# Performance work log

Measured on AMD Instinct MI355X. Metric: run time of the kernel, lower is better.

Reference implementation:

```python
import jax, jax.numpy as jnp
import numpy as np

D_MODEL = 1024
N_HEADS = 16
WINDOW = 256
CAUSAL = True


def build_sliding_window_mask(T, window_size, causal=True):
    half = window_size // 2
    i = jnp.arange(T)[:, None]
    j = jnp.arange(T)[None, :]
    attend = jnp.abs(i - j) <= half
    if causal:
        attend = attend & (j <= i)
    return jnp.where(attend, 0.0, -jnp.inf).astype(jnp.float32)  # (T, T)


def setup_inputs() -> dict:
    key = jax.random.key(0)
    kx, kq, kk, kv, ko = jax.random.split(key, 5)
    B, T, D = 2, 2048, D_MODEL
    s = 1.0 / np.sqrt(D)
    return {
        "x": jax.random.normal(kx, (B, T, D), jnp.float32),
        "Wq": jax.random.normal(kq, (D, D), jnp.float32) * s,
        "Wk": jax.random.normal(kk, (D, D), jnp.float32) * s,
        "Wv": jax.random.normal(kv, (D, D), jnp.float32) * s,
        "Wo": jax.random.normal(ko, (D, D), jnp.float32) * s,
    }


def reference(x, Wq, Wk, Wv, Wo):
    B, T, D = x.shape
    H = N_HEADS
    dh = D // H
    # torch nn.Linear: y = x @ W.T
    def proj(W):
        return (x @ W.T).reshape(B, T, H, dh).transpose(0, 2, 1, 3)  # (B,H,T,dh)

    q, k, v = proj(Wq), proj(Wk), proj(Wv)
    scale = jnp.sqrt(jnp.asarray(dh, x.dtype))
    scores = jnp.einsum("bhtd,bhsd->bhts", q, k) / scale  # (B,H,T,T)
    mask = build_sliding_window_mask(T, WINDOW, CAUSAL)
    scores = scores + mask[None, None]
    attn = jax.nn.softmax(scores, axis=-1)
    attn = jnp.nan_to_num(attn, nan=0.0)
    out = jnp.einsum("bhts,bhsd->bhtd", attn, v)  # (B,H,T,dh)
    out = out.transpose(0, 2, 1, 3).reshape(B, T, D)
    return out @ Wo.T
```

## Files before the change

### kernel.cpp

```cpp
#include <hip/hip_runtime.h>
#include <hip/hip_bf16.h>

#define B_  2
#define T_  2048
#define D_  1024
#define H_  16
#define DH_ 64
#define M_  (B_ * T_)

typedef short s16x8 __attribute__((ext_vector_type(8)));
typedef float f32x4 __attribute__((ext_vector_type(4)));

__device__ inline float bfu(unsigned short u) {
    union { unsigned int i; float f; } c; c.i = ((unsigned int)u) << 16; return c.f;
}
__device__ inline unsigned short f2bf(float f) {
    union { float f; unsigned int i; } c; c.f = f;
    unsigned int r = c.i + 0x7fffu + ((c.i >> 16) & 1u);
    return (unsigned short)(r >> 16);
}
__device__ inline void stv(float* p, float v) { __builtin_nontemporal_store(v, p); }
__device__ inline void stv(unsigned short* p, float v) { *p = f2bf(v); }

__device__ inline void gload_lds16(const unsigned short* g, unsigned short* l) {
    __builtin_amdgcn_global_load_lds(
        (const __attribute__((address_space(1))) void*)g,
        (__attribute__((address_space(3))) void*)l, 16, 0, 0);
}

__global__ __launch_bounds__(256) void conv_bf16(const float* __restrict__ x,
                                                 const float* __restrict__ Wq,
                                                 const float* __restrict__ Wk,
                                                 const float* __restrict__ Wv,
                                                 const float* __restrict__ Wo,
                                                 unsigned short* __restrict__ dst) {
    for (int g = blockIdx.x * 256 + threadIdx.x; g < (1 << 21); g += 2048 * 256) {
        const float* s; size_t o;
        if (g < (1 << 20)) { s = x; o = (size_t)g; }
        else {
            int gg = g - (1 << 20);
            int w = gg >> 18;
            o = (size_t)(gg & ((1 << 18) - 1));
            s = (w == 0) ? Wq : (w == 1) ? Wk : (w == 2) ? Wv : Wo;
        }
        float4 v = ((const float4*)s)[o];
        ushort4 u;
        u.x = f2bf(v.x); u.y = f2bf(v.y); u.z = f2bf(v.z); u.w = f2bf(v.w);
        ((ushort4*)dst)[g] = u;
    }
}

template <int BM, int BN, int NH, typename Tout>
__global__ __launch_bounds__(256, 4) void gemm_m97(const unsigned short* __restrict__ A,
                                                   const unsigned short* __restrict__ Bw,
                                                   Tout* __restrict__ C0,
                                                   Tout* __restrict__ C1,
                                                   unsigned short* __restrict__ vtr,
                                                   int K) {
    constexpr int MI = BM / 32;
    constexpr int NI = BN / 32;
    __shared__ unsigned short As[NH * BM * 32];
    __shared__ unsigned short Bs[NH * BN * 32];
    const int tid  = threadIdx.x;
    const int lane = tid & 63;
    const int wave = tid >> 6;
    const int wr = wave >> 1, wc = wave & 1;

    const int gx  = gridDim.x;
    const int nwg = gx * gridDim.y;
    const int hw  = blockIdx.x + gx * blockIdx.y;
    const int l   = (hw & 7) * (nwg >> 3) + (hw >> 3);
    const int bxl = l % gx, byl = l / gx;
    const int bm = byl * BM, bn = bxl * BN;

    const int fr = lane & 15, kg = lane >> 4;
    const int lrow = lane >> 2;
    const int lcol = (lane & 3) * 8;

    f32x4 acc[MI][NI];
    #pragma unroll
    for (int mi = 0; mi < MI; ++mi)
        #pragma unroll
        for (int ni = 0; ni < NI; ++ni)
            #pragma unroll
            for (int r = 0; r < 4; ++r) acc[mi][ni][r] = 0.f;

    const unsigned short* ga = A  + (size_t)(bm + wave * 16 + lrow) * K + lcol;
    const unsigned short* gb = Bw + (size_t)(bn + wave * 16 + lrow) * K + lcol;
    unsigned short* la = &As[(wave * 16) * 32];
    unsigned short* lb = &Bs[(wave * 16) * 32];

    for (int k0 = 0; k0 < K; k0 += 32 * NH) {
        __syncthreads();
        #pragma unroll
        for (int hf = 0; hf < NH; ++hf) {
            #pragma unroll
            for (int s = 0; s < BM / 64; ++s)
                gload_lds16(ga + k0 + hf * 32 + (size_t)(s * 64) * K,
                            la + hf * BM * 32 + s * 64 * 32);
            #pragma unroll
            for (int s = 0; s < BN / 64; ++s)
                gload_lds16(gb + k0 + hf * 32 + (size_t)(s * 64) * K,
                            lb + hf * BN * 32 + s * 64 * 32);
        }
        __syncthreads();
        #pragma unroll
        for (int hf = 0; hf < NH; ++hf) {
            s16x8 af[MI], bfv[NI];
            #pragma unroll
            for (int mi = 0; mi < MI; ++mi)
                af[mi] = *(const s16x8*)&As[hf * BM * 32 + (wr * (BM / 2) + mi * 16 + fr) * 32 + kg * 8];
            #pragma unroll
            for (int ni = 0; ni < NI; ++ni)
                bfv[ni] = *(const s16x8*)&Bs[hf * BN * 32 + (wc * (BN / 2) + ni * 16 + fr) * 32 + kg * 8];
            #pragma unroll
            for (int mi = 0; mi < MI; ++mi)
                #pragma unroll
                for (int ni = 0; ni < NI; ++ni)
                    acc[mi][ni] = __builtin_amdgcn_mfma_f32_16x16x32_bf16(af[mi], bfv[ni], acc[mi][ni], 0, 0, 0);
        }
    }

    if (vtr && bn >= 2048) {
        #pragma unroll
        for (int mi = 0; mi < MI; ++mi)
            #pragma unroll
            for (int ni = 0; ni < NI; ++ni) {
                const int nl = (bn - 2048) + wc * (BN / 2) + ni * 16 + fr;
                const int h = nl >> 6, d = nl & 63;
                const int m0 = bm + wr * (BM / 2) + mi * 16 + kg * 4;
                const int b = m0 >> 11, t0 = m0 & (T_ - 1);
                ushort4 u;
                u.x = f2bf(acc[mi][ni][0]); u.y = f2bf(acc[mi][ni][1]);
                u.z = f2bf(acc[mi][ni][2]); u.w = f2bf(acc[mi][ni][3]);
                *(ushort4*)(vtr + ((size_t)(b * H_ + h) * 64 + d) * T_ + t0) = u;
            }
        return;
    }
    Tout* C = (bn < 1024) ? C0 : C1;
    const int nb = bn & 1023;
    #pragma unroll
    for (int mi = 0; mi < MI; ++mi)
        #pragma unroll
        for (int ni = 0; ni < NI; ++ni)
            #pragma unroll
            for (int r = 0; r < 4; ++r) {
                int m = bm + wr * (BM / 2) + mi * 16 + kg * 4 + r;
                int n = nb + wc * (BN / 2) + ni * 16 + fr;
                stv(&C[(size_t)m * 1024 + n], acc[mi][ni][r]);
            }
}

__global__ __launch_bounds__(256) void swa_mfma4(const unsigned short* qb,
                                                 const unsigned short* __restrict__ kb,
                                                 const unsigned short* __restrict__ vt,
                                                 unsigned short* ob) {
    __shared__ unsigned short Ks[192 * 64];
    __shared__ unsigned short Vs[64 * 208];
    const int wave = threadIdx.x >> 6;
    const int lane = threadIdx.x & 63;
    const int blk = (blockIdx.x & 7) * 128 + (blockIdx.x >> 3);
    const int i0b = (blk & 31) * 64;
    const int bh  = blk >> 5;
    const int h = bh & (H_ - 1), b = bh >> 4;
    const int g = lane >> 4, l15 = lane & 15;

    const size_t rowbase = (size_t)b * T_ * D_ + (size_t)h * DH_;
    const int klo2 = (i0b > 128) ? (i0b - 128) : 0;

    {
        const int lr = lane >> 3;
        const int gc = (lane & 7) ^ lr;
        const unsigned short* kg0 = kb + rowbase + (size_t)(klo2 + lr) * D_ + gc * 8;
        #pragma unroll
        for (int s = 0; s < 6; ++s) {
            const int i = wave * 6 + s;
            gload_lds16(kg0 + (size_t)(i * 8) * D_, &Ks[i * 8 * 64]);
        }
    }
    {
        const unsigned short* vtb = vt + (size_t)bh * 64 * T_ + klo2;
        #pragma unroll
        for (int s = 0; s < 7; ++s) {
            const int i = s * 4 + wave;
            if (i < 26) {
                const int cc = i * 64 + lane;
                const int d  = cc / 26;
                const int sl = cc - d * 26;
                const int c  = (sl < 24) ? (sl ^ (d & 7)) : sl;
                gload_lds16(vtb + (size_t)d * T_ + c * 8, &Vs[i * 512]);
            }
        }
    }

    const int i0  = i0b + wave * 16;
    const int klo = (i0 > 128) ? (i0 - 128) : 0;
    const int koff = klo - klo2;

    const unsigned short* qrow = qb + rowbase + (size_t)(i0 + l15) * D_ + g * 8;
    const s16x8 aq0 = *(const s16x8*)(qrow);
    const s16x8 aq1 = *(const s16x8*)(qrow + 32);

    __syncthreads();

    f32x4 sacc[9];
    #pragma unroll
    for (int t = 0; t < 9; ++t)
        #pragma unroll
        for (int r = 0; r < 4; ++r) sacc[t][r] = 0.f;

    #pragma unroll
    for (int t = 0; t < 9; ++t) {
        const int row = koff + t * 16 + l15;
        const int r7 = row & 7;
        s16x8 b0 = *(const s16x8*)&Ks[row * 64 + ((g     ^ r7) * 8)];
        s16x8 b1 = *(const s16x8*)&Ks[row * 64 + (((g+4) ^ r7) * 8)];
        __builtin_amdgcn_s_setprio(1);
        sacc[t] = __builtin_amdgcn_mfma_f32_16x16x32_bf16(aq0, b0, sacc[t], 0, 0, 0);
        sacc[t] = __builtin_amdgcn_mfma_f32_16x16x32_bf16(aq1, b1, sacc[t], 0, 0, 0);
        __builtin_amdgcn_s_setprio(0);
    }

    __syncthreads();
    unsigned short* Pw = &Ks[wave * (16 * 168)];
    {
        int row = lane >> 2, col = 144 + (lane & 3) * 4;
        *(uint2*)&Pw[row * 168 + col] = make_uint2(0u, 0u);
    }

    float mrow[4] = {-1e30f, -1e30f, -1e30f, -1e30f};
    #pragma unroll
    for (int t = 0; t < 9; ++t)
        #pragma unroll
        for (int r = 0; r < 4; ++r) {
            const int j  = klo + t * 16 + l15;
            const int iq = i0 + g * 4 + r;
            const bool valid = (j <= iq) && (j + 128 >= iq);
            const float s = valid ? sacc[t][r] * 0.125f : -1e30f;
            sacc[t][r] = s;
            mrow[r] = fmaxf(mrow[r], s);
        }
    #pragma unroll
    for (int r = 0; r < 4; ++r)
        #pragma unroll
        for (int off = 1; off < 16; off <<= 1)
            mrow[r] = fmaxf(mrow[r], __shfl_xor(mrow[r], off));

    float lrow[4] = {0.f, 0.f, 0.f, 0.f};
    #pragma unroll
    for (int t = 0; t < 9; ++t)
        #pragma unroll
        for (int r = 0; r < 4; ++r) {
            const float p = __expf(sacc[t][r] - mrow[r]);
            sacc[t][r] = p;
            lrow[r] += p;
        }
    #pragma unroll
    for (int r = 0; r < 4; ++r) {
        #pragma unroll
        for (int off = 1; off < 16; off <<= 1)
            lrow[r] += __shfl_xor(lrow[r], off);
    }
    float invl[4];
    #pragma unroll
    for (int r = 0; r < 4; ++r) invl[r] = 1.f / lrow[r];

    #pragma unroll
    for (int t = 0; t < 9; ++t)
        #pragma unroll
        for (int r = 0; r < 4; ++r)
            Pw[(g * 4 + r) * 168 + t * 16 + l15] = f2bf(sacc[t][r]);

    f32x4 oacc[4];
    #pragma unroll
    for (int nt = 0; nt < 4; ++nt)
        #pragma unroll
        for (int r = 0; r < 4; ++r) oacc[nt][r] = 0.f;

    const int kc0 = koff >> 3;
    #pragma unroll
    for (int kt = 0; kt < 5; ++kt) {
        const s16x8 ap = *(const s16x8*)&Pw[l15 * 168 + kt * 32 + g * 8];
        s16x8 bvv[4];
        #pragma unroll
        for (int nt = 0; nt < 4; ++nt) {
            const int d = nt * 16 + l15;
            const int c = kc0 + kt * 4 + g;
            const int sl = (c < 24) ? (c ^ (d & 7)) : c;
            bvv[nt] = *(const s16x8*)&Vs[d * 208 + sl * 8];
        }
        __builtin_amdgcn_s_setprio(1);
        #pragma unroll
        for (int nt = 0; nt < 4; ++nt)
            oacc[nt] = __builtin_amdgcn_mfma_f32_16x16x32_bf16(ap, bvv[nt], oacc[nt], 0, 0, 0);
        __builtin_amdgcn_s_setprio(0);
    }

    #pragma unroll
    for (int nt = 0; nt < 4; ++nt)
        #pragma unroll
        for (int r = 0; r < 4; ++r) {
            const float val = oacc[nt][r] * invl[r];
            ob[rowbase + (size_t)(i0 + g * 4 + r) * D_ + nt * 16 + l15] = f2bf(val);
        }
}

extern "C" void kernel_launch(void* const* d_in, const int* in_sizes, int n_in,
                              void* d_out, int out_size, void* d_ws, size_t ws_size,
                              hipStream_t stream) {
    const float* x  = (const float*)d_in[0];
    const float* Wq = (const float*)d_in[1];
    const float* Wk = (const float*)d_in[2];
    const float* Wv = (const float*)d_in[3];
    const float* Wo = (const float*)d_in[4];

    const size_t MD = (size_t)M_ * D_;
    const size_t WN = (size_t)D_ * D_;

    unsigned short* wsb = (unsigned short*)d_ws;
    unsigned short* xb  = wsb;
    unsigned short* Wqb = xb + MD;
    unsigned short* Wob = Wqb + 3 * WN;
    unsigned short* qb  = Wob + WN;
    unsigned short* vt = (unsigned short*)d_out;
    unsigned short* kb = vt + MD;

    conv_bf16<<<2048, 256, 0, stream>>>(x, Wq, Wk, Wv, Wo, wsb);

    gemm_m97<128, 128, 2, unsigned short><<<dim3(24, M_ / 128), 256, 0, stream>>>(
        xb, Wqb, qb, kb, vt, D_);

    swa_mfma4<<<(B_ * H_ * T_) / 64, 256, 0, stream>>>(qb, kb, vt, qb);

    gemm_m97<64, 128, 4, float><<<dim3(8, M_ / 64), 256, 0, stream>>>(
        qb, Wob, (float*)d_out, (float*)d_out, nullptr, D_);
}
```

Measured before the change: 140.2 us.

## Fuse all four stages into one persistent kernel with grid barriers

Replaces the four separate launches (convert, QKV GEMM, sliding-window attention, output GEMM) with one persistent kernel of 768 blocks. The stages are separated by atomic-counter grid barriers, and one shared LDS buffer is reused across stages. This removes per-launch overhead and the gaps between kernels. In exchange it adds a memset, barrier spin cost, and load imbalance, since the attention stage runs 1024 tiles over 768 blocks and the last GEMM uses only 512 blocks. It also relies on all blocks being co-resident, which is checked once through an occupancy query.

```diff
diff --git a/kernel.cpp b/kernel.cpp
--- a/kernel.cpp
+++ b/kernel.cpp
@@ -28,13 +28,27 @@
         (__attribute__((address_space(3))) void*)l, 16, 0, 0);
 }
 
-__global__ __launch_bounds__(256) void conv_bf16(const float* __restrict__ x,
-                                                 const float* __restrict__ Wq,
-                                                 const float* __restrict__ Wk,
-                                                 const float* __restrict__ Wv,
-                                                 const float* __restrict__ Wo,
-                                                 unsigned short* __restrict__ dst) {
-    for (int g = blockIdx.x * 256 + threadIdx.x; g < (1 << 21); g += 2048 * 256) {
+__device__ inline void gridbar(int* c, int nblk) {
+    __syncthreads();
+    __threadfence();
+    if (threadIdx.x == 0) {
+        int t = atomicAdd(c, 1) + 1;
+        int target = ((t + nblk - 1) / nblk) * nblk;
+        while (__hip_atomic_load(c, __ATOMIC_RELAXED, __HIP_MEMORY_SCOPE_AGENT) < target)
+            __builtin_amdgcn_s_sleep(16);
+    }
+    __syncthreads();
+    __threadfence();
+}
+
+__device__ __forceinline__ void conv_work(const float* __restrict__ x,
+                                          const float* __restrict__ Wq,
+                                          const float* __restrict__ Wk,
+                                          const float* __restrict__ Wv,
+                                          const float* __restrict__ Wo,
+                                          unsigned short* __restrict__ dst,
+                                          int nblocks) {
+    for (int g = blockIdx.x * 256 + threadIdx.x; g < (1 << 21); g += nblocks * 256) {
         const float* s; size_t o;
         if (g < (1 << 20)) { s = x; o = (size_t)g; }
         else {
@@ -50,25 +64,29 @@
     }
 }
 
+__global__ __launch_bounds__(256) void conv_bf16(const float* __restrict__ x,
+                                                 const float* __restrict__ Wq,
+                                                 const float* __restrict__ Wk,
+                                                 const float* __restrict__ Wv,
+                                                 const float* __restrict__ Wo,
+                                                 unsigned short* __restrict__ dst) {
+    conv_work(x, Wq, Wk, Wv, Wo, dst, 2048);
+}
+
 template <int BM, int BN, int NH, typename Tout>
-__global__ __launch_bounds__(256, 4) void gemm_m97(const unsigned short* __restrict__ A,
-                                                   const unsigned short* __restrict__ Bw,
-                                                   Tout* __restrict__ C0,
-                                                   Tout* __restrict__ C1,
-                                                   unsigned short* __restrict__ vtr,
-                                                   int K) {
+__device__ __forceinline__ void gemm_tile(unsigned short* As, unsigned short* Bs,
+                                          const unsigned short* __restrict__ A,
+                                          const unsigned short* __restrict__ Bw,
+                                          Tout* __restrict__ C0, Tout* __restrict__ C1,
+                                          unsigned short* __restrict__ vtr, int K,
+                                          int hw, int gx, int nwg) {
     constexpr int MI = BM / 32;
     constexpr int NI = BN / 32;
-    __shared__ unsigned short As[NH * BM * 32];
-    __shared__ unsigned short Bs[NH * BN * 32];
     const int tid  = threadIdx.x;
     const int lane = tid & 63;
     const int wave = tid >> 6;
     const int wr = wave >> 1, wc = wave & 1;
 
-    const int gx  = gridDim.x;
-    const int nwg = gx * gridDim.y;
-    const int hw  = blockIdx.x + gx * blockIdx.y;
     const int l   = (hw & 7) * (nwg >> 3) + (hw >> 3);
     const int bxl = l % gx, byl = l / gx;
     const int bm = byl * BM, bn = bxl * BN;
@@ -151,15 +169,29 @@
             }
 }
 
-__global__ __launch_bounds__(256) void swa_mfma4(const unsigned short* qb,
-                                                 const unsigned short* __restrict__ kb,
-                                                 const unsigned short* __restrict__ vt,
-                                                 unsigned short* ob) {
-    __shared__ unsigned short Ks[192 * 64];
-    __shared__ unsigned short Vs[64 * 208];
+template <int BM, int BN, int NH, typename Tout>
+__global__ __launch_bounds__(256, 4) void gemm_m97(const unsigned short* __restrict__ A,
+                                                   const unsigned short* __restrict__ Bw,
+                                                   Tout* __restrict__ C0,
+                                                   Tout* __restrict__ C1,
+                                                   unsigned short* __restrict__ vtr,
+                                                   int K) {
+    __shared__ __align__(16) unsigned short As[NH * BM * 32];
+    __shared__ __align__(16) unsigned short Bs[NH * BN * 32];
+    gemm_tile<BM, BN, NH, Tout>(As, Bs, A, Bw, C0, C1, vtr, K,
+                                blockIdx.x + gridDim.x * blockIdx.y,
+                                gridDim.x, gridDim.x * gridDim.y);
+}
+
+__device__ __forceinline__ void swa_tile(unsigned short* Ks, unsigned short* Vs,
+                                         const unsigned short* qb,
+                                         const unsigned short* __restrict__ kb,
+                                         const unsigned short* __restrict__ vt,
+                                         unsigned short* ob, int traw) {
+    __syncthreads();
     const int wave = threadIdx.x >> 6;
     const int lane = threadIdx.x & 63;
-    const int blk = (blockIdx.x & 7) * 128 + (blockIdx.x >> 3);
+    const int blk = (traw & 7) * 128 + (traw >> 3);
     const int i0b = (blk & 31) * 64;
     const int bh  = blk >> 5;
     const int h = bh & (H_ - 1), b = bh >> 4;
@@ -305,6 +337,51 @@
         }
 }
 
+__global__ __launch_bounds__(256) void swa_mfma4(const unsigned short* qb,
+                                                 const unsigned short* __restrict__ kb,
+                                                 const unsigned short* __restrict__ vt,
+                                                 unsigned short* ob) {
+    __shared__ __align__(16) unsigned short Ks[192 * 64];
+    __shared__ __align__(16) unsigned short Vs[64 * 208];
+    swa_tile(Ks, Vs, qb, kb, vt, ob, blockIdx.x);
+}
+
+__global__ __launch_bounds__(256, 3) void fused_all(const float* __restrict__ x,
+                                                    const float* __restrict__ Wq,
+                                                    const float* __restrict__ Wk,
+                                                    const float* __restrict__ Wv,
+                                                    const float* __restrict__ Wo,
+                                                    unsigned short* wsb,
+                                                    float* out, int* bar) {
+    __shared__ __align__(16) unsigned short lds[25600];
+    const size_t MD = (size_t)M_ * D_;
+    const size_t WN = (size_t)D_ * D_;
+    unsigned short* xb  = wsb;
+    unsigned short* Wqb = xb + MD;
+    unsigned short* Wob = Wqb + 3 * WN;
+    unsigned short* qb  = Wob + WN;
+    unsigned short* vt = (unsigned short*)out;
+    unsigned short* kb = vt + MD;
+
+    conv_work(x, Wq, Wk, Wv, Wo, wsb, 768);
+    gridbar(&bar[0], 768);
+
+    gemm_tile<128, 128, 2, unsigned short>(lds, lds + 2 * 128 * 32,
+                                           xb, Wqb, qb, kb, vt, D_,
+                                           blockIdx.x, 24, 768);
+    gridbar(&bar[16], 768);
+
+    swa_tile(lds, lds + 192 * 64, qb, kb, vt, qb, blockIdx.x);
+    if (blockIdx.x < 256)
+        swa_tile(lds, lds + 192 * 64, qb, kb, vt, qb, 768 + blockIdx.x);
+    gridbar(&bar[32], 768);
+
+    if (blockIdx.x < 512)
+        gemm_tile<64, 128, 4, float>(lds, lds + 4 * 64 * 32,
+                                     qb, Wob, out, out, nullptr, D_,
+                                     blockIdx.x, 8, 512);
+}
+
 extern "C" void kernel_launch(void* const* d_in, const int* in_sizes, int n_in,
                               void* d_out, int out_size, void* d_ws, size_t ws_size,
                               hipStream_t stream) {
@@ -325,13 +402,25 @@
     unsigned short* vt = (unsigned short*)d_out;
     unsigned short* kb = vt + MD;
 
+    const size_t bar_off = (MD + 4 * WN + MD) * sizeof(unsigned short);
+    static int cap = -1;
+    if (cap < 0) {
+        if (hipOccupancyMaxActiveBlocksPerMultiprocessor(&cap, fused_all, 256, 0)
+            != hipSuccess) cap = 0;
+    }
+
+    if (cap >= 3 && ws_size >= bar_off + 256) {
+        int* bar = (int*)((char*)d_ws + bar_off);
+        hipMemsetAsync(bar, 0, 256, stream);
+        fused_all<<<768, 256, 0, stream>>>(x, Wq, Wk, Wv, Wo, wsb,
+                                           (float*)d_out, bar);
+        return;
+    }
+
     conv_bf16<<<2048, 256, 0, stream>>>(x, Wq, Wk, Wv, Wo, wsb);
-
     gemm_m97<128, 128, 2, unsigned short><<<dim3(24, M_ / 128), 256, 0, stream>>>(
         xb, Wqb, qb, kb, vt, D_);
-
     swa_mfma4<<<(B_ * H_ * T_) / 64, 256, 0, stream>>>(qb, kb, vt, qb);
-
     gemm_m97<64, 128, 4, float><<<dim3(8, M_ / 64), 256, 0, stream>>>(
         qb, Wob, (float*)d_out, (float*)d_out, nullptr, D_);
 }
```

After: 140.0 us. No clear change (-0.1%).
